# Optimization experiments

Measured on AMD Instinct MI355X. Metric: run time of the kernel, lower is better.

The kernel has to match this reference:

```python
import jax, jax.numpy as jnp
import numpy as np

C_Z, H, C = 128, 4, 32
L = 320
SCALE = 1.0 / np.sqrt(C)
EPS = 1e-5


def setup_inputs() -> dict:
    key = jax.random.key(0)
    ks = jax.random.split(key, 8)
    s = 0.02
    return {
        "z": jax.random.normal(ks[0], (L, L, C_Z), dtype=jnp.float32),
        "pair_mask": jnp.ones((L, L), dtype=jnp.float32),
        "res_mask": jnp.ones((L,), dtype=bool),
        "ln_gamma": jnp.ones((C_Z,), dtype=jnp.float32),
        "ln_beta": jnp.zeros((C_Z,), dtype=jnp.float32),
        "Wq": jax.random.normal(ks[1], (C_Z, H * C), dtype=jnp.float32) * s,
        "Wk": jax.random.normal(ks[2], (C_Z, H * C), dtype=jnp.float32) * s,
        "Wv": jax.random.normal(ks[3], (C_Z, H * C), dtype=jnp.float32) * s,
        "Wb": jax.random.normal(ks[4], (C_Z, H), dtype=jnp.float32) * s,
        "Wg": jax.random.normal(ks[5], (C_Z, H * C), dtype=jnp.float32) * s,
        "Wout": jax.random.normal(ks[6], (H * C, C_Z), dtype=jnp.float32) * s,
    }


def _layernorm(x, gamma, beta):
    mu = jnp.mean(x, axis=-1, keepdims=True)
    var = jnp.mean(jnp.square(x - mu), axis=-1, keepdims=True)
    return (x - mu) * jax.lax.rsqrt(var + EPS) * gamma + beta


def reference(z, pair_mask, res_mask, ln_gamma, ln_beta, Wq, Wk, Wv, Wb, Wg, Wout):
    Ldim = z.shape[0]
    z_ln = _layernorm(z, ln_gamma, ln_beta)                      # [L,L,c_z]
    Q = (z_ln @ Wq).reshape(Ldim, Ldim, H, C)                    # [i,j,h,c]
    K = (z_ln @ Wk).reshape(Ldim, Ldim, H, C)                    # [i,k,h,c]
    V = (z_ln @ Wv).reshape(Ldim, Ldim, H, C)                    # [i,k,h,c]
    B = z_ln @ Wb                                                # [j,k,h]
    G = jax.nn.sigmoid(z_ln @ Wg).reshape(Ldim, Ldim, H, C)      # [i,j,h,c]

    # logits[i,h,j,k] = <Q[i,j], K[i,k]> * scale + B[j,k,h]
    logits = jnp.einsum("ijhc,ikhc->ihjk", Q, K) * SCALE
    logits = logits + jnp.transpose(B, (2, 0, 1))[None]          # +[1,h,j,k]
    neg_inf = jnp.asarray(-jnp.inf, logits.dtype)
    logits = jnp.where(res_mask[None, None, None, :], logits, neg_inf)
    attn = jax.nn.softmax(logits, axis=-1)                       # over k

    out = jnp.einsum("ihjk,ikhc->ijhc", attn, V)                 # [i,j,h,c]
    out = (G * out).reshape(Ldim, Ldim, H * C)
    dz = out @ Wout                                              # [L,L,c_z]
    return dz * pair_mask[..., None]
```

## Files before the change

### kernel.cpp

```cpp
#include <hip/hip_runtime.h>

#define LDIM 320
#define CZ 128
#define NH 4
#define CH 32
#define SCALE2F (0.17677669529663687f * 1.4426950408889634f)
#define LOG2E 1.4426950408889634f
#define LN_EPS 1e-5f

typedef __attribute__((ext_vector_type(8))) short bf16x8;
typedef __attribute__((ext_vector_type(4))) float f32x4;

__device__ __forceinline__ unsigned int pack_bf2(float a, float b) {
  unsigned int ua = __float_as_uint(a);
  unsigned int ub = __float_as_uint(b);
  unsigned int ra = (ua + 0x7fffu + ((ua >> 16) & 1u)) >> 16;
  unsigned int rb = (ub + 0x7fffu + ((ub >> 16) & 1u)) >> 16;
  return (ra & 0xffffu) | (rb << 16);
}

__device__ __forceinline__ unsigned short f2bf(float a) {
  unsigned int ua = __float_as_uint(a);
  return (unsigned short)((ua + 0x7fffu + ((ua >> 16) & 1u)) >> 16);
}

__device__ __forceinline__ float bf2f(unsigned short u) {
  return __uint_as_float(((unsigned int)u) << 16);
}

__device__ __forceinline__ unsigned cvtpk(float a, float b) {
  unsigned r;
  asm("v_cvt_pk_bf16_f32 %0, %1, %2" : "=v"(r) : "v"(a), "v"(b));
  return r;
}

__device__ __forceinline__ void plswap(unsigned& a, unsigned& b) {
  asm volatile("v_permlane32_swap_b32 %0, %1" : "+v"(a), "+v"(b));
}

__global__ __launch_bounds__(256) void k_prep(
    const float* __restrict__ Wq, const float* __restrict__ Wk,
    const float* __restrict__ Wv, const float* __restrict__ Wb,
    const float* __restrict__ Wg, const float* __restrict__ Wout,
    unsigned short* __restrict__ Wt, unsigned short* __restrict__ Woutt)
{
  __shared__ __attribute__((aligned(16))) unsigned short buf[64 * 136];
  const int t = threadIdx.x, bid = blockIdx.x;
  const bool isOut = (bid >= 9);
  const int n0 = isOut ? (bid - 9) * 64 : bid * 64;
  const int nl = t & 63;
  const int n = n0 + nl;
#pragma unroll 8
  for (int it = 0; it < 32; ++it) {
    const int k = (t >> 6) + 4 * it;
    float v;
    if (isOut)        v = Wout[k * 128 + n];
    else if (n < 128) v = Wq[k * 128 + n];
    else if (n < 256) v = Wk[k * 128 + n - 128];
    else if (n < 384) v = Wv[k * 128 + n - 256];
    else if (n < 512) v = Wg[k * 128 + n - 384];
    else if (n < 516) v = Wb[k * 4 + n - 512];
    else              v = 0.f;
    buf[nl * 136 + k] = f2bf(v);
  }
  __syncthreads();
  unsigned short* dst = isOut ? Woutt : Wt;
#pragma unroll
  for (int it = 0; it < 4; ++it) {
    const int idx = t + 256 * it;
    const int rr = idx >> 4, ck = idx & 15;
    const uint4 d = *(const uint4*)&buf[rr * 136 + ck * 8];
    *(uint4*)(dst + (size_t)(n0 + rr) * 128 + ck * 8) = d;
  }
}

__global__ __launch_bounds__(256) void k_lnproj(
    const float* __restrict__ z, const float* __restrict__ gamma,
    const float* __restrict__ beta, const unsigned short* __restrict__ Wt,
    const int* __restrict__ rmask,
    unsigned short* __restrict__ Qg, unsigned short* __restrict__ Kg,
    unsigned short* __restrict__ Vg, unsigned short* __restrict__ Gg,
    float* __restrict__ Bh)
{
  __shared__ __attribute__((aligned(16))) unsigned short As[128 * 136];
  const int t = threadIdx.x;
  const int m0 = blockIdx.x * 128;
  const int rlane = t & 7;

  const float* gp = gamma + rlane * 16;
  const float* bp = beta + rlane * 16;
  const float4 g0 = *(const float4*)(gp + 0);
  const float4 g1 = *(const float4*)(gp + 4);
  const float4 g2 = *(const float4*)(gp + 8);
  const float4 g3 = *(const float4*)(gp + 12);
  const float4 b0 = *(const float4*)(bp + 0);
  const float4 b1 = *(const float4*)(bp + 4);
  const float4 b2 = *(const float4*)(bp + 8);
  const float4 b3 = *(const float4*)(bp + 12);

#pragma unroll
  for (int rr = 0; rr < 4; ++rr) {
    const int row = rr * 32 + (t >> 3);
    const float* zp = z + (size_t)(m0 + row) * CZ + rlane * 16;
    const float4 x0 = *(const float4*)(zp + 0);
    const float4 x1 = *(const float4*)(zp + 4);
    const float4 x2 = *(const float4*)(zp + 8);
    const float4 x3 = *(const float4*)(zp + 12);
    float s  = x0.x + x0.y + x0.z + x0.w + x1.x + x1.y + x1.z + x1.w +
               x2.x + x2.y + x2.z + x2.w + x3.x + x3.y + x3.z + x3.w;
    float ss = x0.x*x0.x + x0.y*x0.y + x0.z*x0.z + x0.w*x0.w +
               x1.x*x1.x + x1.y*x1.y + x1.z*x1.z + x1.w*x1.w +
               x2.x*x2.x + x2.y*x2.y + x2.z*x2.z + x2.w*x2.w +
               x3.x*x3.x + x3.y*x3.y + x3.z*x3.z + x3.w*x3.w;
    s  += __shfl_xor(s, 1);  ss += __shfl_xor(ss, 1);
    s  += __shfl_xor(s, 2);  ss += __shfl_xor(ss, 2);
    s  += __shfl_xor(s, 4);  ss += __shfl_xor(ss, 4);
    const float mu  = s * (1.f / 128.f);
    const float var = ss * (1.f / 128.f) - mu * mu;
    const float rs  = rsqrtf(var + LN_EPS);
    uint4 u0, u1;
    u0.x = pack_bf2((x0.x - mu) * rs * g0.x + b0.x, (x0.y - mu) * rs * g0.y + b0.y);
    u0.y = pack_bf2((x0.z - mu) * rs * g0.z + b0.z, (x0.w - mu) * rs * g0.w + b0.w);
    u0.z = pack_bf2((x1.x - mu) * rs * g1.x + b1.x, (x1.y - mu) * rs * g1.y + b1.y);
    u0.w = pack_bf2((x1.z - mu) * rs * g1.z + b1.z, (x1.w - mu) * rs * g1.w + b1.w);
    u1.x = pack_bf2((x2.x - mu) * rs * g2.x + b2.x, (x2.y - mu) * rs * g2.y + b2.y);
    u1.y = pack_bf2((x2.z - mu) * rs * g2.z + b2.z, (x2.w - mu) * rs * g2.w + b2.w);
    u1.z = pack_bf2((x3.x - mu) * rs * g3.x + b3.x, (x3.y - mu) * rs * g3.y + b3.y);
    u1.w = pack_bf2((x3.z - mu) * rs * g3.z + b3.z, (x3.w - mu) * rs * g3.w + b3.w);
    unsigned short* dst = &As[row * 136 + rlane * 16];
    *(uint4*)(dst + 0) = u0;
    *(uint4*)(dst + 8) = u1;
  }
  __syncthreads();

  const int w = t >> 6, lane = t & 63;
  const int m16 = lane & 15, qd = lane >> 4;
  const f32x4 z4 = {0.f, 0.f, 0.f, 0.f};

  bf16x8 af[2][4];
#pragma unroll
  for (int ks = 0; ks < 4; ++ks) {
    af[0][ks] = *(const bf16x8*)&As[(w * 32 + m16) * 136 + ks * 32 + qd * 8];
    af[1][ks] = *(const bf16x8*)&As[(w * 32 + 16 + m16) * 136 + ks * 32 + qd * 8];
  }

  for (int ntile = 0; ntile < 8; ++ntile) {
    f32x4 acc[2][4];
#pragma unroll
    for (int sub = 0; sub < 2; ++sub)
#pragma unroll
      for (int nt = 0; nt < 4; ++nt) acc[sub][nt] = z4;
#pragma unroll
    for (int ks = 0; ks < 4; ++ks) {
#pragma unroll
      for (int nt = 0; nt < 4; ++nt) {
        const bf16x8 bf = *(const bf16x8*)(
            Wt + (size_t)(ntile * 64 + m16 * 4 + nt) * 128 + ks * 32 + qd * 8);
        acc[0][nt] = __builtin_amdgcn_mfma_f32_16x16x32_bf16(af[0][ks], bf, acc[0][nt], 0, 0, 0);
        acc[1][nt] = __builtin_amdgcn_mfma_f32_16x16x32_bf16(af[1][ks], bf, acc[1][nt], 0, 0, 0);
      }
    }
    const int cc0 = (m16 * 4) & 31;
    const int hh = (ntile & 1) * 2 + (m16 >> 3);
    unsigned short* dstb =
        (ntile < 2 ? Qg : (ntile < 4 ? Kg : (ntile < 6 ? Vg : Gg)));
#pragma unroll
    for (int sub = 0; sub < 2; ++sub) {
#pragma unroll
      for (int r = 0; r < 4; ++r) {
        const int p = m0 + w * 32 + sub * 16 + qd * 4 + r;
        const int a = p / 320, bb = p - a * 320;
        float v0 = acc[sub][0][r], v1 = acc[sub][1][r];
        float v2 = acc[sub][2][r], v3 = acc[sub][3][r];
        if (ntile >= 6) {
          v0 = 1.f / (1.f + __expf(-v0));
          v1 = 1.f / (1.f + __expf(-v1));
          v2 = 1.f / (1.f + __expf(-v2));
          v3 = 1.f / (1.f + __expf(-v3));
        }
        uint2 pk;
        pk.x = pack_bf2(v0, v1);
        pk.y = pack_bf2(v2, v3);
        *(uint2*)(dstb + ((size_t)(a * 4 + hh) * 320 + bb) * 32 + cc0) = pk;
      }
    }
  }

  {
    f32x4 acc0 = z4, acc1 = z4;
#pragma unroll
    for (int ks = 0; ks < 4; ++ks) {
      const bf16x8 bf = *(const bf16x8*)(
          Wt + (size_t)(512 + m16) * 128 + ks * 32 + qd * 8);
      acc0 = __builtin_amdgcn_mfma_f32_16x16x32_bf16(af[0][ks], bf, acc0, 0, 0, 0);
      acc1 = __builtin_amdgcn_mfma_f32_16x16x32_bf16(af[1][ks], bf, acc1, 0, 0, 0);
    }
    if (m16 < 4) {
#pragma unroll
      for (int r = 0; r < 4; ++r) {
        const int p0 = m0 + w * 32 + qd * 4 + r;
        const int p1 = p0 + 16;
        const float mk0 = rmask[p0 % 320] ? 0.f : -INFINITY;
        const float mk1 = rmask[p1 % 320] ? 0.f : -INFINITY;
        Bh[(size_t)m16 * 102400 + p0] = acc0[r] * LOG2E + mk0;
        Bh[(size_t)m16 * 102400 + p1] = acc1[r] * LOG2E + mk1;
      }
    }
  }
}

__global__ __launch_bounds__(256) void k_attn(
    const unsigned short* __restrict__ Qg, const unsigned short* __restrict__ Kg,
    const unsigned short* __restrict__ Vg, const unsigned short* __restrict__ Gg,
    const float* __restrict__ Bh, unsigned short* __restrict__ Obg)
{
  __shared__ __attribute__((aligned(16))) unsigned short Vt[32 * 328];
  const int h = blockIdx.x, i = blockIdx.y;
  const int t = threadIdx.x;
  const size_t base = (size_t)(i * NH + h) * (LDIM * CH);

  {
    const int k0 = t >> 3, c4 = (t & 7) * 4;
#pragma unroll
    for (int it = 0; it < 10; ++it) {
      const int k = k0 + 32 * it;
      const uint2 d = *(const uint2*)(Vg + base + k * 32 + c4);
      Vt[(c4 + 0) * 328 + k] = (unsigned short)(d.x & 0xffffu);
      Vt[(c4 + 1) * 328 + k] = (unsigned short)(d.x >> 16);
      Vt[(c4 + 2) * 328 + k] = (unsigned short)(d.y & 0xffffu);
      Vt[(c4 + 3) * 328 + k] = (unsigned short)(d.y >> 16);
    }
  }
  __syncthreads();

  const int w = t >> 6, lane = t & 63;
  const int m16 = lane & 15, qd = lane >> 4;
  const int odd = qd & 1;
  const f32x4 z4 = {0.f, 0.f, 0.f, 0.f};

  for (int jt = w; jt < 20; jt += 4) {
    const bf16x8 qfrag =
        *(const bf16x8*)(Qg + base + (size_t)(jt * 16 + m16) * 32 + qd * 8);

    f32x4 acc[20];
    __builtin_amdgcn_s_setprio(1);
#pragma unroll
    for (int kt = 0; kt < 20; ++kt) {
      const bf16x8 kf =
          *(const bf16x8*)(Kg + base + (size_t)(kt * 16 + m16) * 32 + qd * 8);
      acc[kt] = __builtin_amdgcn_mfma_f32_16x16x32_bf16(kf, qfrag, z4, 0, 0, 0);
    }
    __builtin_amdgcn_s_setprio(0);

    const float* bq = Bh + (size_t)h * 102400 +
                      (size_t)(jt * 16 + m16) * 320 + qd * 4;
    float mxa = -INFINITY, mxb = -INFINITY;
#pragma unroll
    for (int kt = 0; kt < 20; ++kt) {
      const float4 bv = *(const float4*)(bq + kt * 16);
      const float s0 = fmaf(acc[kt][0], SCALE2F, bv.x);
      const float s1 = fmaf(acc[kt][1], SCALE2F, bv.y);
      const float s2 = fmaf(acc[kt][2], SCALE2F, bv.z);
      const float s3 = fmaf(acc[kt][3], SCALE2F, bv.w);
      acc[kt][0] = s0; acc[kt][1] = s1; acc[kt][2] = s2; acc[kt][3] = s3;
      mxa = fmaxf(mxa, fmaxf(s0, s1));
      mxb = fmaxf(mxb, fmaxf(s2, s3));
    }
    float mx = fmaxf(mxa, mxb);
    mx = fmaxf(mx, __shfl_xor(mx, 16));
    mx = fmaxf(mx, __shfl_xor(mx, 32));

    float l0 = 0.f, l1 = 0.f, l2 = 0.f, l3 = 0.f;
#pragma unroll
    for (int kt = 0; kt < 20; ++kt) {
      const float p0 = __builtin_amdgcn_exp2f(acc[kt][0] - mx);
      const float p1 = __builtin_amdgcn_exp2f(acc[kt][1] - mx);
      const float p2 = __builtin_amdgcn_exp2f(acc[kt][2] - mx);
      const float p3 = __builtin_amdgcn_exp2f(acc[kt][3] - mx);
      acc[kt][0] = p0; acc[kt][1] = p1; acc[kt][2] = p2; acc[kt][3] = p3;
      l0 += p0; l1 += p1; l2 += p2; l3 += p3;
    }
    float l = (l0 + l1) + (l2 + l3);
    l += __shfl_xor(l, 16);
    l += __shfl_xor(l, 32);
    const float rl = __builtin_amdgcn_rcpf(l);
    float rle[4];
#pragma unroll
    for (int r = 0; r < 4; ++r) rle[r] = __shfl(rl, qd * 4 + r);

    f32x4 accO0 = z4, accO1 = z4;
#pragma unroll
    for (int hh = 0; hh < 2; ++hh) {
      unsigned Wl[10], Wh[10];
#pragma unroll
      for (int kr = 0; kr < 10; ++kr) {
        Wl[kr] = cvtpk(acc[hh * 10 + kr][0], acc[hh * 10 + kr][1]);
        Wh[kr] = cvtpk(acc[hh * 10 + kr][2], acc[hh * 10 + kr][3]);
      }
      __builtin_amdgcn_s_setprio(1);
#pragma unroll
      for (int ks = 0; ks < 5; ++ks) {
        unsigned a0 = Wl[2 * ks], b0 = Wl[2 * ks + 1];
        plswap(a0, b0);
        const unsigned c0 = __shfl_xor(a0, 16), d0 = __shfl_xor(b0, 16);
        unsigned a1 = Wh[2 * ks], b1 = Wh[2 * ks + 1];
        plswap(a1, b1);
        const unsigned c1 = __shfl_xor(a1, 16), d1 = __shfl_xor(b1, 16);
        union { unsigned u[4]; bf16x8 v; } fr;
        fr.u[0] = odd ? d0 : a0;
        fr.u[1] = odd ? d1 : a1;
        fr.u[2] = odd ? b0 : c0;
        fr.u[3] = odd ? b1 : c1;
        const bf16x8 v0 =
            *(const bf16x8*)&Vt[m16 * 328 + hh * 160 + ks * 32 + qd * 8];
        const bf16x8 v1 =
            *(const bf16x8*)&Vt[(16 + m16) * 328 + hh * 160 + ks * 32 + qd * 8];
        accO0 = __builtin_amdgcn_mfma_f32_16x16x32_bf16(fr.v, v0, accO0, 0, 0, 0);
        accO1 = __builtin_amdgcn_mfma_f32_16x16x32_bf16(fr.v, v1, accO1, 0, 0, 0);
      }
      __builtin_amdgcn_s_setprio(0);
    }

#pragma unroll
    for (int r = 0; r < 4; ++r) {
      const int j = jt * 16 + qd * 4 + r;
      const float g0 = bf2f(Gg[base + (size_t)j * 32 + m16]);
      const float g1 = bf2f(Gg[base + (size_t)j * 32 + 16 + m16]);
      unsigned short* op = Obg + (size_t)(i * 320 + j) * 128 + h * 32;
      op[m16]      = f2bf(g0 * rle[r] * accO0[r]);
      op[16 + m16] = f2bf(g1 * rle[r] * accO1[r]);
    }
  }
}

__global__ __launch_bounds__(256) void k_out(
    const unsigned short* __restrict__ Obg, const unsigned short* __restrict__ Woutt,
    const float* __restrict__ pm, float* __restrict__ out)
{
  __shared__ __attribute__((aligned(16))) unsigned short As[128 * 136];
  __shared__ __attribute__((aligned(16))) unsigned short Bs[64 * 136];
  const int t = threadIdx.x;
  const int ntile = blockIdx.x;
  const int m0 = blockIdx.y * 128;

#pragma unroll
  for (int it = 0; it < 8; ++it) {
    const int idx = t + 256 * it;
    const int rr = idx >> 4, ck = idx & 15;
    const uint4 d = *(const uint4*)(Obg + (size_t)(m0 + rr) * 128 + ck * 8);
    *(uint4*)&As[rr * 136 + ck * 8] = d;
  }
  {
    const unsigned short* wrow = Woutt + (size_t)ntile * 64 * 128;
#pragma unroll
    for (int it = 0; it < 4; ++it) {
      const int idx = t + 256 * it;
      const int n = idx >> 4, ck = idx & 15;
      const uint4 d = *(const uint4*)(wrow + n * 128 + ck * 8);
      *(uint4*)&Bs[n * 136 + ck * 8] = d;
    }
  }
  __syncthreads();

  const int w = t >> 6, lane = t & 63;
  const int m16 = lane & 15, qd = lane >> 4;
  const f32x4 z4 = {0.f, 0.f, 0.f, 0.f};
  f32x4 acc[2][4];
#pragma unroll
  for (int sub = 0; sub < 2; ++sub)
#pragma unroll
    for (int nt = 0; nt < 4; ++nt) acc[sub][nt] = z4;

#pragma unroll
  for (int ks = 0; ks < 4; ++ks) {
    const bf16x8 af0 = *(const bf16x8*)&As[(w * 32 + m16) * 136 + qd * 8 + ks * 32];
    const bf16x8 af1 = *(const bf16x8*)&As[(w * 32 + 16 + m16) * 136 + qd * 8 + ks * 32];
#pragma unroll
    for (int nt = 0; nt < 4; ++nt) {
      const bf16x8 bf = *(const bf16x8*)&Bs[(nt * 16 + m16) * 136 + qd * 8 + ks * 32];
      acc[0][nt] = __builtin_amdgcn_mfma_f32_16x16x32_bf16(af0, bf, acc[0][nt], 0, 0, 0);
      acc[1][nt] = __builtin_amdgcn_mfma_f32_16x16x32_bf16(af1, bf, acc[1][nt], 0, 0, 0);
    }
  }

#pragma unroll
  for (int sub = 0; sub < 2; ++sub) {
#pragma unroll
    for (int r = 0; r < 4; ++r) {
      const int p = m0 + w * 32 + sub * 16 + qd * 4 + r;
      const float m = pm[p];
      float* orow = out + (size_t)p * 128 + ntile * 64;
#pragma unroll
      for (int nt = 0; nt < 4; ++nt)
        orow[nt * 16 + m16] = acc[sub][nt][r] * m;
    }
  }
}

extern "C" void kernel_launch(void* const* d_in, const int* in_sizes, int n_in,
                              void* d_out, int out_size, void* d_ws, size_t ws_size,
                              hipStream_t stream)
{
  const float* z     = (const float*)d_in[0];
  const float* pmask = (const float*)d_in[1];
  const int*   rmask = (const int*)d_in[2];
  const float* gamma = (const float*)d_in[3];
  const float* beta  = (const float*)d_in[4];
  const float* Wq    = (const float*)d_in[5];
  const float* Wk    = (const float*)d_in[6];
  const float* Wv    = (const float*)d_in[7];
  const float* Wb    = (const float*)d_in[8];
  const float* Wg    = (const float*)d_in[9];
  const float* Wout  = (const float*)d_in[10];

  const size_t P = (size_t)LDIM * LDIM;
  const size_t E = P * 128;
  char* ws = (char*)d_ws;
  unsigned short* Qg = (unsigned short*)ws;
  unsigned short* Kg = Qg + E;
  unsigned short* Vg = Kg + E;
  unsigned short* Gg = Vg + E;
  unsigned short* Obg = Gg + E;
  unsigned short* Wt = Obg + E;
  unsigned short* Woutt = Wt + 576 * 128;
  float* Bh = (float*)(Woutt + 128 * 128);

  k_prep<<<dim3(11), 256, 0, stream>>>(Wq, Wk, Wv, Wb, Wg, Wout, Wt, Woutt);
  k_lnproj<<<dim3(800), 256, 0, stream>>>(z, gamma, beta, Wt, rmask,
                                          Qg, Kg, Vg, Gg, Bh);
  k_attn<<<dim3(NH, LDIM), 256, 0, stream>>>(Qg, Kg, Vg, Gg, Bh, Obg);
  k_out<<<dim3(2, 800), 256, 0, stream>>>(Obg, Woutt, pmask, (float*)d_out);
}
```

Measured before the change: 362.5 us.

## Stage softmax probabilities through LDS and swap MFMA operands for vectorized output

```diff
diff --git a/kernel.cpp b/kernel.cpp
--- a/kernel.cpp
+++ b/kernel.cpp
@@ -32,10 +32,6 @@
   unsigned r;
   asm("v_cvt_pk_bf16_f32 %0, %1, %2" : "=v"(r) : "v"(a), "v"(b));
   return r;
-}
-
-__device__ __forceinline__ void plswap(unsigned& a, unsigned& b) {
-  asm volatile("v_permlane32_swap_b32 %0, %1" : "+v"(a), "+v"(b));
 }
 
 __global__ __launch_bounds__(256) void k_prep(
@@ -215,6 +211,7 @@
     const float* __restrict__ Bh, unsigned short* __restrict__ Obg)
 {
   __shared__ __attribute__((aligned(16))) unsigned short Vt[32 * 328];
+  __shared__ __attribute__((aligned(16))) unsigned short Ps[4][16 * 168];
   const int h = blockIdx.x, i = blockIdx.y;
   const int t = threadIdx.x;
   const size_t base = (size_t)(i * NH + h) * (LDIM * CH);
@@ -235,7 +232,6 @@
 
   const int w = t >> 6, lane = t & 63;
   const int m16 = lane & 15, qd = lane >> 4;
-  const int odd = qd & 1;
   const f32x4 z4 = {0.f, 0.f, 0.f, 0.f};
 
   for (int jt = w; jt < 20; jt += 4) {
@@ -254,7 +250,7 @@
 
     const float* bq = Bh + (size_t)h * 102400 +
                       (size_t)(jt * 16 + m16) * 320 + qd * 4;
-    float mxa = -INFINITY, mxb = -INFINITY;
+    float mx[4] = {-INFINITY, -INFINITY, -INFINITY, -INFINITY};
 #pragma unroll
     for (int kt = 0; kt < 20; ++kt) {
       const float4 bv = *(const float4*)(bq + kt * 16);
@@ -263,20 +259,22 @@
       const float s2 = fmaf(acc[kt][2], SCALE2F, bv.z);
       const float s3 = fmaf(acc[kt][3], SCALE2F, bv.w);
       acc[kt][0] = s0; acc[kt][1] = s1; acc[kt][2] = s2; acc[kt][3] = s3;
-      mxa = fmaxf(mxa, fmaxf(s0, s1));
-      mxb = fmaxf(mxb, fmaxf(s2, s3));
-    }
-    float mx = fmaxf(mxa, mxb);
-    mx = fmaxf(mx, __shfl_xor(mx, 16));
-    mx = fmaxf(mx, __shfl_xor(mx, 32));
+      mx[0] = fmaxf(mx[0], s0);
+      mx[1] = fmaxf(mx[1], s1);
+      mx[2] = fmaxf(mx[2], s2);
+      mx[3] = fmaxf(mx[3], s3);
+    }
+    float mxx = fmaxf(fmaxf(mx[0], mx[1]), fmaxf(mx[2], mx[3]));
+    mxx = fmaxf(mxx, __shfl_xor(mxx, 16));
+    mxx = fmaxf(mxx, __shfl_xor(mxx, 32));
 
     float l0 = 0.f, l1 = 0.f, l2 = 0.f, l3 = 0.f;
 #pragma unroll
     for (int kt = 0; kt < 20; ++kt) {
-      const float p0 = __builtin_amdgcn_exp2f(acc[kt][0] - mx);
-      const float p1 = __builtin_amdgcn_exp2f(acc[kt][1] - mx);
-      const float p2 = __builtin_amdgcn_exp2f(acc[kt][2] - mx);
-      const float p3 = __builtin_amdgcn_exp2f(acc[kt][3] - mx);
+      const float p0 = __builtin_amdgcn_exp2f(acc[kt][0] - mxx);
+      const float p1 = __builtin_amdgcn_exp2f(acc[kt][1] - mxx);
+      const float p2 = __builtin_amdgcn_exp2f(acc[kt][2] - mxx);
+      const float p3 = __builtin_amdgcn_exp2f(acc[kt][3] - mxx);
       acc[kt][0] = p0; acc[kt][1] = p1; acc[kt][2] = p2; acc[kt][3] = p3;
       l0 += p0; l1 += p1; l2 += p2; l3 += p3;
     }
@@ -284,51 +282,52 @@
     l += __shfl_xor(l, 16);
     l += __shfl_xor(l, 32);
     const float rl = __builtin_amdgcn_rcpf(l);
-    float rle[4];
-#pragma unroll
-    for (int r = 0; r < 4; ++r) rle[r] = __shfl(rl, qd * 4 + r);
 
     f32x4 accO0 = z4, accO1 = z4;
 #pragma unroll
     for (int hh = 0; hh < 2; ++hh) {
-      unsigned Wl[10], Wh[10];
-#pragma unroll
-      for (int kr = 0; kr < 10; ++kr) {
-        Wl[kr] = cvtpk(acc[hh * 10 + kr][0], acc[hh * 10 + kr][1]);
-        Wh[kr] = cvtpk(acc[hh * 10 + kr][2], acc[hh * 10 + kr][3]);
+#pragma unroll
+      for (int kt2 = 0; kt2 < 10; ++kt2) {
+        const int kt = hh * 10 + kt2;
+        uint2 wv;
+        wv.x = cvtpk(acc[kt][0], acc[kt][1]);
+        wv.y = cvtpk(acc[kt][2], acc[kt][3]);
+        *(uint2*)&Ps[w][m16 * 168 + kt2 * 16 + qd * 4] = wv;
       }
       __builtin_amdgcn_s_setprio(1);
 #pragma unroll
       for (int ks = 0; ks < 5; ++ks) {
-        unsigned a0 = Wl[2 * ks], b0 = Wl[2 * ks + 1];
-        plswap(a0, b0);
-        const unsigned c0 = __shfl_xor(a0, 16), d0 = __shfl_xor(b0, 16);
-        unsigned a1 = Wh[2 * ks], b1 = Wh[2 * ks + 1];
-        plswap(a1, b1);
-        const unsigned c1 = __shfl_xor(a1, 16), d1 = __shfl_xor(b1, 16);
-        union { unsigned u[4]; bf16x8 v; } fr;
-        fr.u[0] = odd ? d0 : a0;
-        fr.u[1] = odd ? d1 : a1;
-        fr.u[2] = odd ? b0 : c0;
-        fr.u[3] = odd ? b1 : c1;
+        const bf16x8 pf = *(const bf16x8*)&Ps[w][m16 * 168 + ks * 32 + qd * 8];
         const bf16x8 v0 =
             *(const bf16x8*)&Vt[m16 * 328 + hh * 160 + ks * 32 + qd * 8];
         const bf16x8 v1 =
             *(const bf16x8*)&Vt[(16 + m16) * 328 + hh * 160 + ks * 32 + qd * 8];
-        accO0 = __builtin_amdgcn_mfma_f32_16x16x32_bf16(fr.v, v0, accO0, 0, 0, 0);
-        accO1 = __builtin_amdgcn_mfma_f32_16x16x32_bf16(fr.v, v1, accO1, 0, 0, 0);
+        accO0 = __builtin_amdgcn_mfma_f32_16x16x32_bf16(v0, pf, accO0, 0, 0, 0);
+        accO1 = __builtin_amdgcn_mfma_f32_16x16x32_bf16(v1, pf, accO1, 0, 0, 0);
       }
       __builtin_amdgcn_s_setprio(0);
     }
 
-#pragma unroll
-    for (int r = 0; r < 4; ++r) {
-      const int j = jt * 16 + qd * 4 + r;
-      const float g0 = bf2f(Gg[base + (size_t)j * 32 + m16]);
-      const float g1 = bf2f(Gg[base + (size_t)j * 32 + 16 + m16]);
+    {
+      const int j = jt * 16 + m16;
+      const uint2 gg0 = *(const uint2*)(Gg + base + (size_t)j * 32 + qd * 4);
+      const uint2 gg1 = *(const uint2*)(Gg + base + (size_t)j * 32 + 16 + qd * 4);
+      const float ga0 = bf2f((unsigned short)(gg0.x & 0xffffu));
+      const float ga1 = bf2f((unsigned short)(gg0.x >> 16));
+      const float ga2 = bf2f((unsigned short)(gg0.y & 0xffffu));
+      const float ga3 = bf2f((unsigned short)(gg0.y >> 16));
+      const float gb0 = bf2f((unsigned short)(gg1.x & 0xffffu));
+      const float gb1 = bf2f((unsigned short)(gg1.x >> 16));
+      const float gb2 = bf2f((unsigned short)(gg1.y & 0xffffu));
+      const float gb3 = bf2f((unsigned short)(gg1.y >> 16));
       unsigned short* op = Obg + (size_t)(i * 320 + j) * 128 + h * 32;
-      op[m16]      = f2bf(g0 * rle[r] * accO0[r]);
-      op[16 + m16] = f2bf(g1 * rle[r] * accO1[r]);
+      uint2 o0, o1;
+      o0.x = cvtpk(ga0 * rl * accO0[0], ga1 * rl * accO0[1]);
+      o0.y = cvtpk(ga2 * rl * accO0[2], ga3 * rl * accO0[3]);
+      o1.x = cvtpk(gb0 * rl * accO1[0], gb1 * rl * accO1[1]);
+      o1.y = cvtpk(gb2 * rl * accO1[2], gb3 * rl * accO1[3]);
+      *(uint2*)(op + qd * 4) = o0;
+      *(uint2*)(op + 16 + qd * 4) = o1;
     }
   }
 }
```

Measured after the change: 340.7 us. -6.0%, faster.
